# Performance work log

Hardware: AMD Instinct MI355X
Metric: run time of the kernel (lower is better)

## Reference

```python
import jax, jax.numpy as jnp
import numpy as np

B, C, H, W = 2, 512, 64, 64
GROUPS = 32
EPS = 1e-6


def setup_inputs() -> dict:
    key = jax.random.key(0)
    ks = jax.random.split(key, 9)
    s = 1.0 / np.sqrt(C)
    return {
        "x": jax.random.normal(ks[0], (B, C, H, W), dtype=jnp.float32),
        "gamma": jnp.ones((C,), dtype=jnp.float32),
        "beta": jnp.zeros((C,), dtype=jnp.float32),
        "wq": jax.random.normal(ks[1], (C, C), dtype=jnp.float32) * s,
        "bq": jnp.zeros((C,), dtype=jnp.float32),
        "wk": jax.random.normal(ks[2], (C, C), dtype=jnp.float32) * s,
        "bk": jnp.zeros((C,), dtype=jnp.float32),
        "wv": jax.random.normal(ks[3], (C, C), dtype=jnp.float32) * s,
        "bv": jnp.zeros((C,), dtype=jnp.float32),
        "wp": jax.random.normal(ks[4], (C, C), dtype=jnp.float32) * s,
        "bp": jnp.zeros((C,), dtype=jnp.float32),
    }


def _group_norm(x, gamma, beta):
    b, c, h, w = x.shape
    xg = x.reshape(b, GROUPS, c // GROUPS, h, w)
    mean = jnp.mean(xg, axis=(2, 3, 4), keepdims=True)
    var = jnp.var(xg, axis=(2, 3, 4), keepdims=True)
    xn = ((xg - mean) * jax.lax.rsqrt(var + EPS)).reshape(b, c, h, w)
    return xn * gamma[None, :, None, None] + beta[None, :, None, None]


def reference(x, gamma, beta, wq, bq, wk, bk, wv, bv, wp, bp):
    b, c, h, w = x.shape
    hn = _group_norm(x, gamma, beta)
    # 1x1 convs == per-pixel linear; flatten spatial: (b, hw, c)
    t = hn.reshape(b, c, h * w).transpose(0, 2, 1)
    q = jnp.einsum('bnc,oc->bno', t, wq) + bq
    k = jnp.einsum('bnc,oc->bno', t, wk) + bk
    v = jnp.einsum('bnc,oc->bno', t, wv) + bv
    scale = float(int(c) ** (-0.5))
    attn = jax.nn.softmax(jnp.einsum('bic,bjc->bij', q, k) * scale, axis=-1)
    o = jnp.einsum('bij,bjc->bic', attn, v)  # (b, hw, c)
    o = jnp.einsum('bnc,oc->bno', o, wp) + bp
    o = o.transpose(0, 2, 1).reshape(b, c, h, w)
    return x + o
```

## Files before the change

kernel.cpp:

```cpp
#include <hip/hip_runtime.h>
#include <hip/hip_bf16.h>

#define B_ 2
#define C_ 512
#define HW_ 4096
#define K_ 512
#define EPS_ 1e-6f
#define SCALE_ 0.04419417382415922f
#define NEG_INF_ (-1e30f)

typedef __attribute__((ext_vector_type(8))) __bf16 bf16x8;
typedef __attribute__((ext_vector_type(4))) float f32x4;
typedef __attribute__((ext_vector_type(16))) float f32x16;

__device__ __forceinline__ unsigned short f2bf(float f) {
  union { float f; unsigned u; } v; v.f = f;
  unsigned r = v.u + 0x7fffu + ((v.u >> 16) & 1u);
  return (unsigned short)(r >> 16);
}
__device__ __forceinline__ float bf2f(unsigned short h) {
  union { unsigned u; float f; } v; v.u = ((unsigned)h) << 16;
  return v.f;
}

__device__ __forceinline__ void gld_lds16(const unsigned short* g, unsigned short* l) {
  __builtin_amdgcn_global_load_lds((const __attribute__((address_space(1))) void*)g,
                                   (__attribute__((address_space(3))) void*)l, 16, 0, 0);
}

__global__ void gn_cast(const float* __restrict__ x, float* __restrict__ pstats,
                        const float* __restrict__ s0, const float* __restrict__ s1,
                        const float* __restrict__ s2, const float* __restrict__ s3,
                        unsigned short* __restrict__ dst) {
  int bid = blockIdx.x;
  int t = threadIdx.x;
  if (bid < 1024) {
    int bg = bid >> 4, row = bid & 15;
    int b = bg >> 5, g = bg & 31;
    const float* base = x + ((size_t)(b * C_ + g * 16 + row)) * HW_;
    float s = 0.f, s2 = 0.f;
    #pragma unroll
    for (int i = 0; i < 4; ++i) {
      float4 v = *reinterpret_cast<const float4*>(base + (size_t)(t + i * 256) * 4);
      s  += v.x + v.y + v.z + v.w;
      s2 += v.x * v.x + v.y * v.y + v.z * v.z + v.w * v.w;
    }
    for (int off = 32; off; off >>= 1) { s += __shfl_down(s, off); s2 += __shfl_down(s2, off); }
    __shared__ float rs[4], rs2[4];
    int w = t >> 6;
    if ((t & 63) == 0) { rs[w] = s; rs2[w] = s2; }
    __syncthreads();
    if (t == 0) {
      pstats[bid] = rs[0] + rs[1] + rs[2] + rs[3];
      pstats[1024 + bid] = rs2[0] + rs2[1] + rs2[2] + rs2[3];
    }
  } else {
    int cid = bid - 1024;
    int which = cid >> 8, bx = cid & 255;
    const float* src = which == 0 ? s0 : which == 1 ? s1 : which == 2 ? s2 : s3;
    int i = (bx * 256 + t) * 4;
    float4 v = *reinterpret_cast<const float4*>(src + i);
    ushort4 o; o.x = f2bf(v.x); o.y = f2bf(v.y); o.z = f2bf(v.z); o.w = f2bf(v.w);
    *reinterpret_cast<ushort4*>(dst + (size_t)which * 262144 + i) = o;
  }
}

__global__ void build_t(const float* __restrict__ x, const float* __restrict__ pstats,
                        const float* __restrict__ gamma, const float* __restrict__ beta,
                        unsigned short* __restrict__ tb) {
  __shared__ float lds[64 * 69];
  int n0 = blockIdx.x * 64, c0 = blockIdx.y * 64, b = blockIdx.z;
  int t = threadIdx.x;
  {
    int cl = t >> 2, ch = t & 3;
    int c = c0 + cl;
    int bg = b * 32 + (c >> 4);
    float s = 0.f, s2v = 0.f;
    #pragma unroll
    for (int r = 0; r < 16; ++r) {
      s   += pstats[bg * 16 + r];
      s2v += pstats[1024 + bg * 16 + r];
    }
    float mean = s * (1.f / 65536.f);
    float var = s2v * (1.f / 65536.f) - mean * mean;
    float rstd = rsqrtf(var + EPS_);
    float ga = gamma[c] * rstd;
    float be = beta[c] - mean * ga;
    const float* xr = x + ((size_t)(b * C_ + c)) * HW_ + n0 + ch * 16;
    #pragma unroll
    for (int i = 0; i < 4; ++i) {
      float4 v = *reinterpret_cast<const float4*>(xr + i * 4);
      int nl = ch * 16 + i * 4;
      lds[cl * 69 + nl + 0] = v.x * ga + be;
      lds[cl * 69 + nl + 1] = v.y * ga + be;
      lds[cl * 69 + nl + 2] = v.z * ga + be;
      lds[cl * 69 + nl + 3] = v.w * ga + be;
    }
  }
  __syncthreads();
  {
    int nl = t >> 2, cw = t & 3;
    unsigned short* orow = tb + ((size_t)(b * HW_ + n0 + nl)) * C_ + c0 + cw * 16;
    #pragma unroll
    for (int i = 0; i < 4; ++i) {
      ushort4 o4;
      o4.x = f2bf(lds[(cw * 16 + i * 4 + 0) * 69 + nl]);
      o4.y = f2bf(lds[(cw * 16 + i * 4 + 1) * 69 + nl]);
      o4.z = f2bf(lds[(cw * 16 + i * 4 + 2) * 69 + nl]);
      o4.w = f2bf(lds[(cw * 16 + i * 4 + 3) * 69 + nl]);
      *reinterpret_cast<ushort4*>(orow + i * 4) = o4;
    }
  }
}

__global__ __launch_bounds__(256, 2) void gemm_qkv(
    const unsigned short* __restrict__ tb, const unsigned short* __restrict__ wqkv,
    const float* __restrict__ bq, const float* __restrict__ bk, const float* __restrict__ bv,
    unsigned short* __restrict__ qb, unsigned short* __restrict__ kb,
    unsigned short* __restrict__ vTb) {
  __shared__ unsigned short Al[2][128 * 64];
  __shared__ unsigned short Bl[2][128 * 64];
  int f = blockIdx.x + 4 * (blockIdx.y + 32 * blockIdx.z);
  int xcd = f & 7, i = f >> 3;
  int bx = i & 3;
  int g = xcd * 24 + (i >> 2);
  int bz = g >> 5, by = g & 31;
  int which = bz >> 1, b = bz & 1;
  const unsigned short* Ab = (which < 2) ? (tb + (size_t)b * HW_ * K_) : (wqkv + 2 * 262144);
  const unsigned short* Bb = (which < 2) ? (wqkv + which * 262144) : (tb + (size_t)b * HW_ * K_);
  int m0 = (which < 2) ? by * 128 : bx * 128;
  int n0 = (which < 2) ? bx * 128 : by * 128;
  int N = (which < 2) ? 512 : HW_;
  unsigned short* Cb = (which == 0) ? (qb + (size_t)b * HW_ * K_)
                     : (which == 1) ? (kb + (size_t)b * HW_ * K_)
                                    : (vTb + (size_t)b * C_ * HW_);
  const float* bias = (which == 0) ? bq : (which == 1) ? bk : bv;
  int t = threadIdx.x, lane = t & 63, w = t >> 6;
  int l15 = lane & 15, quad = lane >> 4;
  int mw = (w & 1) * 64, nw = (w >> 1) * 64;
  int sr8 = lane >> 3, sb = lane & 7;
  f32x4 acc[4][4] = {};

  #define G_STAGE(KC) do {                                                          \
    int pb = (KC) & 1;                                                              \
    _Pragma("unroll")                                                               \
    for (int q = 0; q < 4; ++q) {                                                   \
      int row = w * 32 + q * 8 + sr8;                                               \
      int gb = sb ^ (row & 7);                                                      \
      gld_lds16(Ab + (size_t)(m0 + row) * K_ + (KC) * 64 + gb * 8, &Al[pb][(w * 32 + q * 8) * 64]); \
      gld_lds16(Bb + (size_t)(n0 + row) * K_ + (KC) * 64 + gb * 8, &Bl[pb][(w * 32 + q * 8) * 64]); \
    }                                                                               \
  } while (0)

  G_STAGE(0);
  __syncthreads();
  for (int kc = 0; kc < 8; ++kc) {
    if (kc < 7) G_STAGE(kc + 1);
    const unsigned short* Ac = Al[kc & 1];
    const unsigned short* Bc = Bl[kc & 1];
    #pragma unroll
    for (int kk = 0; kk < 2; ++kk) {
      bf16x8 af[4];
      #pragma unroll
      for (int mt = 0; mt < 4; ++mt)
        af[mt] = *reinterpret_cast<const bf16x8*>(
            &Ac[(mw + mt * 16 + l15) * 64 + (((kk * 4 + quad) ^ (l15 & 7)) << 3)]);
      #pragma unroll
      for (int nt = 0; nt < 4; ++nt) {
        bf16x8 bfr = *reinterpret_cast<const bf16x8*>(
            &Bc[(nw + nt * 16 + l15) * 64 + (((kk * 4 + quad) ^ (l15 & 7)) << 3)]);
        #pragma unroll
        for (int mt = 0; mt < 4; ++mt)
          acc[mt][nt] = __builtin_amdgcn_mfma_f32_16x16x32_bf16(af[mt], bfr, acc[mt][nt], 0, 0, 0);
      }
    }
    __syncthreads();
  }
  #undef G_STAGE
  #pragma unroll
  for (int mt = 0; mt < 4; ++mt)
    #pragma unroll
    for (int nt = 0; nt < 4; ++nt)
      #pragma unroll
      for (int rr = 0; rr < 4; ++rr) {
        int row = m0 + mw + mt * 16 + quad * 4 + rr;
        int col = n0 + nw + nt * 16 + l15;
        float v = acc[mt][nt][rr] + ((which < 2) ? bias[col] : bias[row]);
        Cb[(size_t)row * N + col] = f2bf(v);
      }
}

__global__ __launch_bounds__(256, 2) void gemm_fin(
    const unsigned short* __restrict__ A,
    const unsigned short* __restrict__ opart,
    const float* __restrict__ mpart, const float* __restrict__ lpart,
    const float* __restrict__ bias, const float* __restrict__ resid,
    float* __restrict__ out) {
  __shared__ unsigned short Al[2][128 * 64];
  __shared__ unsigned short Bl[2][64 * 68];
  int z = blockIdx.z;
  int n0 = blockIdx.x * 64, m0 = blockIdx.y * 128;
  int t = threadIdx.x, lane = t & 63, w = t >> 6;
  int l15 = lane & 15, quad = lane >> 4;
  int mw = (w & 1) * 64, nw = (w >> 1) * 32;
  int sr8 = lane >> 3, sb = lane & 7;
  f32x4 acc[4][2] = {};

  float w0[2], w1[2];
  int nrow[2];
  #pragma unroll
  for (int q = 0; q < 2; ++q) {
    int n = n0 + w * 16 + q * 8 + sr8;
    nrow[q] = n;
    float ma = mpart[(size_t)z * HW_ + n], mb = mpart[(size_t)(2 + z) * HW_ + n];
    float la = lpart[(size_t)z * HW_ + n], lb = lpart[(size_t)(2 + z) * HW_ + n];
    float M = fmaxf(ma, mb);
    float ea = __expf(ma - M), eb = __expf(mb - M);
    float iv = 1.f / (la * ea + lb * eb);
    w0[q] = ea * iv; w1[q] = eb * iv;
  }
  const unsigned short* p0 = opart + (size_t)z * HW_ * 512;
  const unsigned short* p1 = opart + (size_t)(2 + z) * HW_ * 512;

  #define STAGE_A(KC) do {                                                          \
    int pb = (KC) & 1;                                                              \
    _Pragma("unroll")                                                               \
    for (int q = 0; q < 4; ++q) {                                                   \
      int row = w * 32 + q * 8 + sr8;                                               \
      int gb = sb ^ (row & 7);                                                      \
      gld_lds16(A + (size_t)(m0 + row) * K_ + (KC) * 64 + gb * 8, &Al[pb][(w * 32 + q * 8) * 64]); \
    }                                                                               \
  } while (0)

  #define STAGE_B(KC) do {                                                          \
    int pb = (KC) & 1;                                                              \
    _Pragma("unroll")                                                               \
    for (int q = 0; q < 2; ++q) {                                                   \
      int row = w * 16 + q * 8 + sr8;                                               \
      size_t goff = (size_t)nrow[q] * 512 + (KC) * 64 + sb * 8;                     \
      uint4 u0 = *reinterpret_cast<const uint4*>(p0 + goff);                        \
      uint4 u1 = *reinterpret_cast<const uint4*>(p1 + goff);                        \
      uint4 o4;                                                                     \
      unsigned* a0 = reinterpret_cast<unsigned*>(&u0);                              \
      unsigned* a1 = reinterpret_cast<unsigned*>(&u1);                              \
      unsigned* od = reinterpret_cast<unsigned*>(&o4);                              \
      _Pragma("unroll")                                                             \
      for (int j = 0; j < 4; ++j) {                                                 \
        float lo = bf2f((unsigned short)(a0[j] & 0xffffu)) * w0[q]                  \
                 + bf2f((unsigned short)(a1[j] & 0xffffu)) * w1[q];                 \
        float hi = bf2f((unsigned short)(a0[j] >> 16)) * w0[q]                      \
                 + bf2f((unsigned short)(a1[j] >> 16)) * w1[q];                     \
        od[j] = (unsigned)f2bf(lo) | ((unsigned)f2bf(hi) << 16);                    \
      }                                                                             \
      *reinterpret_cast<uint4*>(&Bl[pb][row * 68 + sb * 8]) = o4;                   \
    }                                                                               \
  } while (0)

  STAGE_A(0);
  STAGE_B(0);
  __syncthreads();
  for (int kc = 0; kc < 8; ++kc) {
    if (kc < 7) { STAGE_A(kc + 1); STAGE_B(kc + 1); }
    const unsigned short* Ac = Al[kc & 1];
    const unsigned short* Bc = Bl[kc & 1];
    #pragma unroll
    for (int kk = 0; kk < 2; ++kk) {
      bf16x8 af[4];
      #pragma unroll
      for (int mt = 0; mt < 4; ++mt)
        af[mt] = *reinterpret_cast<const bf16x8*>(
            &Ac[(mw + mt * 16 + l15) * 64 + (((kk * 4 + quad) ^ (l15 & 7)) << 3)]);
      #pragma unroll
      for (int nt = 0; nt < 2; ++nt) {
        bf16x8 bfr = *reinterpret_cast<const bf16x8*>(
            &Bc[(nw + nt * 16 + l15) * 68 + ((kk * 4 + quad) << 3)]);
        #pragma unroll
        for (int mt = 0; mt < 4; ++mt)
          acc[mt][nt] = __builtin_amdgcn_mfma_f32_16x16x32_bf16(af[mt], bfr, acc[mt][nt], 0, 0, 0);
      }
    }
    __syncthreads();
  }
  #undef STAGE_A
  #undef STAGE_B
  #pragma unroll
  for (int mt = 0; mt < 4; ++mt)
    #pragma unroll
    for (int nt = 0; nt < 2; ++nt)
      #pragma unroll
      for (int rr = 0; rr < 4; ++rr) {
        int row = m0 + mw + mt * 16 + quad * 4 + rr;
        int col = n0 + nw + nt * 16 + l15;
        size_t idx = (size_t)z * (C_ * HW_) + (size_t)row * HW_ + col;
        out[idx] = acc[mt][nt][rr] + bias[row] + resid[idx];
      }
}

__global__ __launch_bounds__(512, 2) void attn(
    const unsigned short* __restrict__ qg, const unsigned short* __restrict__ kg,
    const unsigned short* __restrict__ vg,
    unsigned short* __restrict__ opart, float* __restrict__ mpart, float* __restrict__ lpart) {
  __shared__ unsigned short KVb[2 * 16384];
  __shared__ unsigned short Pl[64 * 264];
  __shared__ float sm_m[64], sm_l[64], sm_alpha[64], sm_red[128];
  int qt = blockIdx.x, jh = blockIdx.y, b = blockIdx.z;
  int t = threadIdx.x, lane = t & 63, w = t >> 6;
  int l15 = lane & 15, quad = lane >> 4;
  int l31 = lane & 31, hl = lane >> 5;
  int rw = w & 3, cw = w >> 2;
  int rw2 = w & 1, dg = w >> 1;
  int m0 = qt * 64;
  if (t < 64) { sm_m[t] = NEG_INF_; sm_l[t] = 0.f; }

  int st_r[4], st_kb[4];
  #pragma unroll
  for (int q = 0; q < 4; ++q) {
    int blk = w * 4 + q;
    st_r[q] = blk * 4 + (lane >> 4);
    st_kb[q] = (lane & 15) ^ (st_r[q] & 7);
  }

  #define STAGE_K(JC, KC, J0) do {                                                  \
    const unsigned short* gb = kg + ((size_t)(b * HW_ + (J0) + (JC) * 128)) * K_ + (KC) * 128; \
    unsigned short* lb = KVb + ((((JC) * 4 + (KC)) & 1) << 14);                     \
    _Pragma("unroll")                                                               \
    for (int q = 0; q < 4; ++q)                                                     \
      gld_lds16(gb + (size_t)st_r[q] * K_ + st_kb[q] * 8, lb + (w * 4 + q) * 512);  \
  } while (0)

  #define STAGE_V(DC, JC, J0) do {                                                 \
    const unsigned short* gb = vg + ((size_t)(b * K_ + (DC) * 128)) * HW_ + (J0) + (JC) * 128; \
    unsigned short* lb = KVb + (((DC) & 1) << 14);                                  \
    _Pragma("unroll")                                                               \
    for (int q = 0; q < 4; ++q)                                                     \
      gld_lds16(gb + (size_t)st_r[q] * HW_ + st_kb[q] * 8, lb + (w * 4 + q) * 512); \
  } while (0)

  bf16x8 qa[16];
  {
    const unsigned short* qrow = qg + ((size_t)(b * HW_ + m0 + rw * 16 + l15)) * K_ + quad * 8;
    #pragma unroll
    for (int kk = 0; kk < 16; ++kk)
      qa[kk] = *reinterpret_cast<const bf16x8*>(qrow + kk * 32);
  }
  f32x16 acc_o[4] = {};

  int j0 = jh * 2048;
  STAGE_K(0, 0, j0);
  __syncthreads();

  for (int it = 0; it < 8; ++it, j0 += 256) {
    f32x4 acc_s[8] = {};
    #pragma unroll
    for (int c = 0; c < 8; ++c) {
      int jc = c >> 2, kc = c & 3;
      if (c < 7) { STAGE_K((c + 1) >> 2, (c + 1) & 3, j0); }
      else       { STAGE_V(0, 0, j0); }
      const unsigned short* bufc = KVb + ((c & 1) << 14);
      __builtin_amdgcn_s_setprio(1);
      #pragma unroll
      for (int kk = 0; kk < 4; ++kk)
        #pragma unroll
        for (int ct = 0; ct < 4; ++ct) {
          int jr = cw * 64 + ct * 16 + l15;
          bf16x8 bfr = *reinterpret_cast<const bf16x8*>(
              &bufc[jr * 128 + (((kk * 4 + quad) ^ (l15 & 7)) << 3)]);
          acc_s[jc * 4 + ct] = __builtin_amdgcn_mfma_f32_16x16x32_bf16(qa[kc * 4 + kk], bfr, acc_s[jc * 4 + ct], 0, 0, 0);
        }
      __builtin_amdgcn_s_setprio(0);
      __syncthreads();
    }
    float mx[4];
    #pragma unroll
    for (int rr = 0; rr < 4; ++rr) {
      float m = NEG_INF_;
      #pragma unroll
      for (int s = 0; s < 8; ++s) {
        acc_s[s][rr] *= SCALE_;
        m = fmaxf(m, acc_s[s][rr]);
      }
      mx[rr] = m;
    }
    #pragma unroll
    for (int off = 1; off < 16; off <<= 1)
      #pragma unroll
      for (int rr = 0; rr < 4; ++rr)
        mx[rr] = fmaxf(mx[rr], __shfl_xor(mx[rr], off));
    if (l15 == 0)
      #pragma unroll
      for (int rr = 0; rr < 4; ++rr)
        sm_red[cw * 64 + rw * 16 + quad * 4 + rr] = mx[rr];
    __syncthreads();
    if (t < 64) {
      float mnew = fmaxf(sm_m[t], fmaxf(sm_red[t], sm_red[64 + t]));
      sm_alpha[t] = __expf(sm_m[t] - mnew);
      sm_m[t] = mnew;
    }
    __syncthreads();
    float sum[4] = {0.f, 0.f, 0.f, 0.f};
    #pragma unroll
    for (int s = 0; s < 8; ++s)
      #pragma unroll
      for (int rr = 0; rr < 4; ++rr) {
        int rowl = rw * 16 + quad * 4 + rr;
        float p = __expf(acc_s[s][rr] - sm_m[rowl]);
        sum[rr] += p;
        Pl[rowl * 264 + (s >> 2) * 128 + cw * 64 + (s & 3) * 16 + l15] = f2bf(p);
      }
    #pragma unroll
    for (int off = 1; off < 16; off <<= 1)
      #pragma unroll
      for (int rr = 0; rr < 4; ++rr)
        sum[rr] += __shfl_xor(sum[rr], off);
    if (l15 == 0)
      #pragma unroll
      for (int rr = 0; rr < 4; ++rr)
        sm_red[cw * 64 + rw * 16 + quad * 4 + rr] = sum[rr];
    __syncthreads();
    if (t < 64)
      sm_l[t] = sm_l[t] * sm_alpha[t] + sm_red[t] + sm_red[64 + t];
    #pragma unroll
    for (int r16 = 0; r16 < 16; ++r16) {
      int row = rw2 * 32 + (r16 & 3) + 8 * (r16 >> 2) + 4 * hl;
      float a = sm_alpha[row];
      #pragma unroll
      for (int dc = 0; dc < 4; ++dc)
        acc_o[dc][r16] *= a;
    }
    bf16x8 pa_r[8];
    #pragma unroll
    for (int c = 0; c < 8; ++c) {
      int jc = c >> 2, dc = c & 3;
      if ((c & 3) == 0) {
        #pragma unroll
        for (int ksx = 0; ksx < 8; ++ksx)
          pa_r[ksx] = *reinterpret_cast<const bf16x8*>(
              &Pl[(rw2 * 32 + l31) * 264 + jc * 128 + ksx * 16 + hl * 8]);
      }
      if (c < 7)          { STAGE_V((c + 1) & 3, (c + 1) >> 2, j0); }
      else if (it < 7)    { STAGE_K(0, 0, j0 + 256); }
      const unsigned short* bufc = KVb + ((c & 1) << 14);
      __builtin_amdgcn_s_setprio(1);
      #pragma unroll
      for (int ksx = 0; ksx < 8; ++ksx) {
        bf16x8 vb = *reinterpret_cast<const bf16x8*>(
            &bufc[(dg * 32 + l31) * 128 + (((ksx * 2 + hl) ^ (l31 & 7)) << 3)]);
        acc_o[dc] = __builtin_amdgcn_mfma_f32_32x32x16_bf16(pa_r[ksx], vb, acc_o[dc], 0, 0, 0);
      }
      __builtin_amdgcn_s_setprio(0);
      __syncthreads();
    }
  }
  #undef STAGE_K
  #undef STAGE_V
  int part = jh * 2 + b;
  unsigned short* ob = opart + ((size_t)part * HW_ + m0) * 512;
  #pragma unroll
  for (int dc = 0; dc < 4; ++dc) {
    int d = dc * 128 + dg * 32 + l31;
    #pragma unroll
    for (int r16 = 0; r16 < 16; ++r16) {
      int row = rw2 * 32 + (r16 & 3) + 8 * (r16 >> 2) + 4 * hl;
      ob[(size_t)row * 512 + d] = f2bf(acc_o[dc][r16]);
    }
  }
  if (t < 64) {
    mpart[(size_t)part * HW_ + m0 + t] = sm_m[t];
    lpart[(size_t)part * HW_ + m0 + t] = sm_l[t];
  }
}

extern "C" void kernel_launch(void* const* d_in, const int* in_sizes, int n_in,
                              void* d_out, int out_size, void* d_ws, size_t ws_size,
                              hipStream_t stream) {
  const float* x     = (const float*)d_in[0];
  const float* gamma = (const float*)d_in[1];
  const float* beta  = (const float*)d_in[2];
  const float* wq    = (const float*)d_in[3];
  const float* bq    = (const float*)d_in[4];
  const float* wk    = (const float*)d_in[5];
  const float* bk    = (const float*)d_in[6];
  const float* wv    = (const float*)d_in[7];
  const float* bv    = (const float*)d_in[8];
  const float* wp    = (const float*)d_in[9];
  const float* bp    = (const float*)d_in[10];
  float* out = (float*)d_out;

  char* ws = (char*)d_ws;
  size_t o = 0;
  float* pstats         = (float*)(ws + o);          o += 8192;
  unsigned short* tb    = (unsigned short*)(ws + o); o += 8388608;
  unsigned short* qb    = (unsigned short*)(ws + o); o += 8388608;
  unsigned short* kb    = (unsigned short*)(ws + o); o += 8388608;
  unsigned short* vTb   = (unsigned short*)(ws + o); o += 8388608;
  unsigned short* wqb   = (unsigned short*)(ws + o); o += 524288;
  unsigned short* wkb   = (unsigned short*)(ws + o); o += 524288;
  unsigned short* wvb   = (unsigned short*)(ws + o); o += 524288;
  unsigned short* wpb   = (unsigned short*)(ws + o); o += 524288;
  unsigned short* opart = (unsigned short*)(ws + o); o += 16777216;
  float* mpart          = (float*)(ws + o);          o += 65536;
  float* lpart          = (float*)(ws + o);          o += 65536;

  gn_cast<<<2048, 256, 0, stream>>>(x, pstats, wq, wk, wv, wp, wqb);
  build_t<<<dim3(64, 8, 2), 256, 0, stream>>>(x, pstats, gamma, beta, tb);
  gemm_qkv<<<dim3(4, 32, 6), 256, 0, stream>>>(tb, wqb, bq, bk, bv, qb, kb, vTb);
  attn<<<dim3(64, 2, 2), 512, 0, stream>>>(qb, kb, vTb, opart, mpart, lpart);
  gemm_fin<<<dim3(64, 4, 2), 256, 0, stream>>>(wpb, opart, mpart, lpart, bp, x, out);
}
```

Baseline: 259.2 us.

## Deepen attention K/V staging to a four-buffer ring and halve block barriers

The shared K/V staging area grows from two to four 16K-element buffers. Each even step now issues loads for the next two chunks, so a block barrier is needed only after every second chunk instead of after every chunk, in both the QK and PV loops. To make room in LDS, the P tile is halved to 128 columns: the second half of the softmax probabilities is recomputed (exp again) and written mid-PV loop, after the first half has been consumed. This trades extra exp work and higher LDS use (about 145KB per block) for fewer syncs and more load latency hiding.

```diff
diff --git a/kernel.cpp b/kernel.cpp
--- a/kernel.cpp
+++ b/kernel.cpp
@@ -300,8 +300,8 @@
     const unsigned short* __restrict__ qg, const unsigned short* __restrict__ kg,
     const unsigned short* __restrict__ vg,
     unsigned short* __restrict__ opart, float* __restrict__ mpart, float* __restrict__ lpart) {
-  __shared__ unsigned short KVb[2 * 16384];
-  __shared__ unsigned short Pl[64 * 264];
+  __shared__ unsigned short KVb[4 * 16384];
+  __shared__ unsigned short Pl[64 * 136];
   __shared__ float sm_m[64], sm_l[64], sm_alpha[64], sm_red[128];
   int qt = blockIdx.x, jh = blockIdx.y, b = blockIdx.z;
   int t = threadIdx.x, lane = t & 63, w = t >> 6;
@@ -320,17 +320,17 @@
     st_kb[q] = (lane & 15) ^ (st_r[q] & 7);
   }
 
-  #define STAGE_K(JC, KC, J0) do {                                                  \
+  #define STAGE_K(JC, KC, J0, BUF) do {                                             \
     const unsigned short* gb = kg + ((size_t)(b * HW_ + (J0) + (JC) * 128)) * K_ + (KC) * 128; \
-    unsigned short* lb = KVb + ((((JC) * 4 + (KC)) & 1) << 14);                     \
+    unsigned short* lb = KVb + ((BUF) << 14);                                       \
     _Pragma("unroll")                                                               \
     for (int q = 0; q < 4; ++q)                                                     \
       gld_lds16(gb + (size_t)st_r[q] * K_ + st_kb[q] * 8, lb + (w * 4 + q) * 512);  \
   } while (0)
 
-  #define STAGE_V(DC, JC, J0) do {                                                 \
+  #define STAGE_V(DC, JC, J0, BUF) do {                                             \
     const unsigned short* gb = vg + ((size_t)(b * K_ + (DC) * 128)) * HW_ + (J0) + (JC) * 128; \
-    unsigned short* lb = KVb + (((DC) & 1) << 14);                                  \
+    unsigned short* lb = KVb + ((BUF) << 14);                                       \
     _Pragma("unroll")                                                               \
     for (int q = 0; q < 4; ++q)                                                     \
       gld_lds16(gb + (size_t)st_r[q] * HW_ + st_kb[q] * 8, lb + (w * 4 + q) * 512); \
@@ -346,17 +346,25 @@
   f32x16 acc_o[4] = {};
 
   int j0 = jh * 2048;
-  STAGE_K(0, 0, j0);
+  STAGE_K(0, 0, j0, 0);
+  STAGE_K(0, 1, j0, 1);
   __syncthreads();
 
   for (int it = 0; it < 8; ++it, j0 += 256) {
     f32x4 acc_s[8] = {};
     #pragma unroll
     for (int c = 0; c < 8; ++c) {
+      if ((c & 1) == 0) {
+        if (c < 6) {
+          STAGE_K((c + 2) >> 2, (c + 2) & 3, j0, (c + 2) & 3);
+          STAGE_K((c + 3) >> 2, (c + 3) & 3, j0, (c + 3) & 3);
+        } else {
+          STAGE_V(0, 0, j0, 0);
+          STAGE_V(1, 0, j0, 1);
+        }
+      }
+      const unsigned short* bufc = KVb + ((c & 3) << 14);
       int jc = c >> 2, kc = c & 3;
-      if (c < 7) { STAGE_K((c + 1) >> 2, (c + 1) & 3, j0); }
-      else       { STAGE_V(0, 0, j0); }
-      const unsigned short* bufc = KVb + ((c & 1) << 14);
       __builtin_amdgcn_s_setprio(1);
       #pragma unroll
       for (int kk = 0; kk < 4; ++kk)
@@ -368,7 +376,7 @@
           acc_s[jc * 4 + ct] = __builtin_amdgcn_mfma_f32_16x16x32_bf16(qa[kc * 4 + kk], bfr, acc_s[jc * 4 + ct], 0, 0, 0);
         }
       __builtin_amdgcn_s_setprio(0);
-      __syncthreads();
+      if (c & 1) __syncthreads();
     }
     float mx[4];
     #pragma unroll
@@ -405,7 +413,8 @@
         int rowl = rw * 16 + quad * 4 + rr;
         float p = __expf(acc_s[s][rr] - sm_m[rowl]);
         sum[rr] += p;
-        Pl[rowl * 264 + (s >> 2) * 128 + cw * 64 + (s & 3) * 16 + l15] = f2bf(p);
+        if (s < 4)
+          Pl[rowl * 136 + cw * 64 + (s & 3) * 16 + l15] = f2bf(p);
       }
     #pragma unroll
     for (int off = 1; off < 16; off <<= 1)
@@ -430,16 +439,33 @@
     bf16x8 pa_r[8];
     #pragma unroll
     for (int c = 0; c < 8; ++c) {
-      int jc = c >> 2, dc = c & 3;
+      if (c == 2) {
+        #pragma unroll
+        for (int s = 4; s < 8; ++s)
+          #pragma unroll
+          for (int rr = 0; rr < 4; ++rr) {
+            int rowl = rw * 16 + quad * 4 + rr;
+            Pl[rowl * 136 + cw * 64 + (s & 3) * 16 + l15] =
+                f2bf(__expf(acc_s[s][rr] - sm_m[rowl]));
+          }
+      }
       if ((c & 3) == 0) {
         #pragma unroll
         for (int ksx = 0; ksx < 8; ++ksx)
           pa_r[ksx] = *reinterpret_cast<const bf16x8*>(
-              &Pl[(rw2 * 32 + l31) * 264 + jc * 128 + ksx * 16 + hl * 8]);
-      }
-      if (c < 7)          { STAGE_V((c + 1) & 3, (c + 1) >> 2, j0); }
-      else if (it < 7)    { STAGE_K(0, 0, j0 + 256); }
-      const unsigned short* bufc = KVb + ((c & 1) << 14);
+              &Pl[(rw2 * 32 + l31) * 136 + ksx * 16 + hl * 8]);
+      }
+      if ((c & 1) == 0) {
+        if (c < 6) {
+          STAGE_V((c + 2) & 3, (c + 2) >> 2, j0, (c + 2) & 3);
+          STAGE_V((c + 3) & 3, (c + 3) >> 2, j0, (c + 3) & 3);
+        } else if (it < 7) {
+          STAGE_K(0, 0, j0 + 256, 0);
+          STAGE_K(0, 1, j0 + 256, 1);
+        }
+      }
+      const unsigned short* bufc = KVb + ((c & 3) << 14);
+      int dc = c & 3;
       __builtin_amdgcn_s_setprio(1);
       #pragma unroll
       for (int ksx = 0; ksx < 8; ++ksx) {
@@ -448,7 +474,7 @@
         acc_o[dc] = __builtin_amdgcn_mfma_f32_32x32x16_bf16(pa_r[ksx], vb, acc_o[dc], 0, 0, 0);
       }
       __builtin_amdgcn_s_setprio(0);
-      __syncthreads();
+      if (c & 1) __syncthreads();
     }
   }
   #undef STAGE_K
```

Measured after the change: 249.5 us. 3.7% less time.
